# Kernel optimization log

Hardware: AMD Instinct MI355X
Metric: run time of the kernel (lower is better)

Reference implementation:

```python
import jax, jax.numpy as jnp
from jax import lax
import numpy as np

B, T, I, H = 256, 1024, 128, 256


def setup_inputs() -> dict:
    key = jax.random.key(0)
    k1, k2, k3 = jax.random.split(key, 3)
    # Xavier-ish scaling so sigmoid/tanh gates are not saturated
    s_ih = float(np.sqrt(2.0 / (I + 3 * H)))
    s_hh = float(np.sqrt(2.0 / (H + 3 * H)))
    return {
        "x": jax.random.normal(k1, (B, T, I), dtype=jnp.float32),
        "h0": jnp.zeros((B, H), dtype=jnp.float32),
        "weight_ih": jax.random.normal(k2, (3 * H, I), dtype=jnp.float32) * s_ih,
        "weight_hh": jax.random.normal(k3, (3 * H, H), dtype=jnp.float32) * s_hh,
        "bias_ih": jnp.zeros((3 * H,), dtype=jnp.float32),
        "bias_hh": jnp.zeros((3 * H,), dtype=jnp.float32),
    }


def reference(x, h0, weight_ih, weight_hh, bias_ih, bias_hh):
    # Precompute batched input-to-hidden GEMM for all timesteps: [B, T, 3H]
    gates_x = jnp.einsum("bti,gi->btg", x, weight_ih) + bias_ih
    gates_x = jnp.swapaxes(gates_x, 0, 1)  # [T, B, 3H] for scan

    def step(h, gx):
        # NOTE: faithful to source — reset gate multiplies the FULL new-gate
        # preactivation (which already includes the hidden contribution),
        # unlike a standard GRU.
        gates = gx + h @ weight_hh.T + bias_hh  # [B, 3H]
        r, z, n = jnp.split(gates, 3, axis=-1)
        r = jax.nn.sigmoid(r)
        z = jax.nn.sigmoid(z)
        n = jnp.tanh(r * n)
        h_new = (1.0 - z) * h + z * n
        return h_new, h_new

    h_last, outs = lax.scan(step, h0, gates_x)  # outs: [T, B, H]
    output = jnp.swapaxes(outs, 0, 1)  # [B, T, H] (batch_first=True)
    return output, h_last
```

## Files before the change

kernel.cpp:

```cpp
#include <hip/hip_runtime.h>


#define B_SZ 256
#define T_SZ 1024
#define H_SZ 256
#define G3   768
#define NGRP 64
#define SPIN_MAX (1 << 27)
#define HROW 288

typedef __attribute__((ext_vector_type(2))) float f32x2;

template<int CTRL>
__device__ __forceinline__ float dppx(float s) {
    return __int_as_float(
        __builtin_amdgcn_update_dpp(0, __float_as_int(s), CTRL, 0xF, 0xF, true));
}
template<int MASK>
__device__ __forceinline__ float swzx(float s) {
    return __int_as_float(__builtin_amdgcn_ds_swizzle(__float_as_int(s), MASK));
}
__device__ __forceinline__ f32x2 pkfma(f32x2 a, f32x2 b, f32x2 c) {
    f32x2 d;
    asm("v_pk_fma_f32 %0, %1, %2, %3" : "=v"(d) : "v"(a), "v"(b), "v"(c));
    return d;
}

static __device__ __forceinline__ int hpos(int k) { return k + 4 * (k >> 5); }

static __device__ __forceinline__ size_t xsl(int g, int par, int n, int u) {
    return (((size_t)g * 2 + par) * 4 + n) * 256 + u;
}

__global__ void prep_kernel(const float* __restrict__ h0,
                            unsigned long long* __restrict__ xch) {
    int tid = blockIdx.x * blockDim.x + threadIdx.x;
    if (tid < B_SZ * H_SZ) {
        int b = tid >> 8, u = tid & 255;
        int g = b >> 2, n = b & 3;
        unsigned long long val = (unsigned long long)__float_as_uint(h0[tid]);
        xch[xsl(g, 0, n, u)] = val;
        xch[xsl(g, 1, n, u)] = val;
    }
}

__global__ __launch_bounds__(256) void gemm_x_kernel(
    const float* __restrict__ x, const float* __restrict__ wih,
    float* __restrict__ gx, int c, int tcShift)
{
    __shared__ __align__(16) float xs[64][132];
    __shared__ __align__(16) float ws[128][68];
    const int TC = 1 << tcShift;
    const int t  = threadIdx.x;
    const int bx = blockIdx.x, by = blockIdx.y;

#pragma unroll
    for (int i = 0; i < 8; ++i) {
        int f4 = t + i * 256;
        int r  = f4 >> 5, c4 = (f4 & 31) * 4;
        int rho = bx * 64 + r;
        int b = rho >> tcShift, u = rho & (TC - 1);
        float4 v = *(const float4*)(x + ((size_t)b * T_SZ + (size_t)c * TC + u) * 128 + c4);
        *(float4*)&xs[r][c4] = v;
    }

    const int gl = t & 31;
    const int rl = t >> 5;
    float acc[8][4];
#pragma unroll
    for (int i = 0; i < 8; ++i)
#pragma unroll
        for (int jj = 0; jj < 4; ++jj) acc[i][jj] = 0.f;

    for (int kb = 0; kb < 2; ++kb) {
        __syncthreads();
#pragma unroll
        for (int i = 0; i < 8; ++i) {
            int f4 = t + i * 256;
            int row = f4 >> 4, c4 = (f4 & 15) * 4;
            float4 v = *(const float4*)(wih + (size_t)(by * 128 + row) * 128 + kb * 64 + c4);
            *(float4*)&ws[row][c4] = v;
        }
        __syncthreads();

#pragma unroll 4
        for (int k4 = 0; k4 < 16; ++k4) {
            float4 wv0 = *(const float4*)&ws[gl     ][k4 * 4];
            float4 wv1 = *(const float4*)&ws[gl + 32][k4 * 4];
            float4 wv2 = *(const float4*)&ws[gl + 64][k4 * 4];
            float4 wv3 = *(const float4*)&ws[gl + 96][k4 * 4];
#pragma unroll
            for (int rr = 0; rr < 8; ++rr) {
                float4 xv = *(const float4*)&xs[rl + rr * 8][kb * 64 + k4 * 4];
                acc[rr][0] = fmaf(xv.w, wv0.w, fmaf(xv.z, wv0.z, fmaf(xv.y, wv0.y, fmaf(xv.x, wv0.x, acc[rr][0]))));
                acc[rr][1] = fmaf(xv.w, wv1.w, fmaf(xv.z, wv1.z, fmaf(xv.y, wv1.y, fmaf(xv.x, wv1.x, acc[rr][1]))));
                acc[rr][2] = fmaf(xv.w, wv2.w, fmaf(xv.z, wv2.z, fmaf(xv.y, wv2.y, fmaf(xv.x, wv2.x, acc[rr][2]))));
                acc[rr][3] = fmaf(xv.w, wv3.w, fmaf(xv.z, wv3.z, fmaf(xv.y, wv3.y, fmaf(xv.x, wv3.x, acc[rr][3]))));
            }
        }
    }

#pragma unroll
    for (int rr = 0; rr < 8; ++rr) {
        size_t base = (size_t)(bx * 64 + rl + rr * 8) * G3 + by * 128 + gl;
#pragma unroll
        for (int gi = 0; gi < 4; ++gi)
            gx[base + 32 * gi] = acc[rr][gi];
    }
}

#define PIN2(v) asm volatile("" : "+v"(v));

__global__ __launch_bounds__(512)
__attribute__((amdgpu_waves_per_eu(2, 2)))
void gru_kernel(
    const float* __restrict__ gx, const float* __restrict__ whh,
    const float* __restrict__ bih, const float* __restrict__ bhh,
    unsigned long long* __restrict__ xch, float* __restrict__ out,
    int gbase, int tc, int isLast)
{
    __shared__ __align__(16) float hl[4][HROW];
    __shared__ __align__(16) float hst[4][64];

    const int t   = threadIdx.x;
    const int bid = blockIdx.x;
    const int g   = bid & 63;
    const int m   = bid >> 6;
    const int u0  = m * 64;
    const int q   = t >> 5;
    const int p   = t & 31;
    const int pb  = p & 3;
    const int uq  = u0 + 4 * q;
    const int k0  = 8 * p;

    f32x2 wf[12][4];
#pragma unroll
    for (int gate = 0; gate < 3; ++gate) {
#pragma unroll
        for (int e = 0; e < 4; ++e) {
            const float* wr = whh + (size_t)(gate * 256 + uq + e) * H_SZ + k0;
            float4 va = *(const float4*)(wr);
            float4 vb = *(const float4*)(wr + 4);
            wf[gate * 4 + e][0] = (f32x2){va.x, va.y};
            wf[gate * 4 + e][1] = (f32x2){va.z, va.w};
            wf[gate * 4 + e][2] = (f32x2){vb.x, vb.y};
            wf[gate * 4 + e][3] = (f32x2){vb.z, vb.w};
        }
    }
#pragma unroll
    for (int f = 0; f < 12; ++f) {
        PIN2(wf[f][0]) PIN2(wf[f][1]) PIN2(wf[f][2]) PIN2(wf[f][3])
    }

    const bool hi  = (p >= 16);
    const bool act = (p < 4) || (p >= 16 && p < 20);
    const int  ueA = uq + (hi ? 2 : 0);
    float bsrA = 0.f, bszA = 0.f, bsnA = 0.f, bsrB = 0.f, bszB = 0.f, bsnB = 0.f;
    const float* gxp = nullptr;
    if (act) {
        bsrA = bih[ueA]       + bhh[ueA];
        bszA = bih[256 + ueA] + bhh[256 + ueA];
        bsnA = bih[512 + ueA] + bhh[512 + ueA];
        bsrB = bih[ueA + 1]       + bhh[ueA + 1];
        bszB = bih[257 + ueA]     + bhh[257 + ueA];
        bsnB = bih[513 + ueA]     + bhh[513 + ueA];
        gxp = gx + ((size_t)(4 * g + pb) * tc) * G3 + ueA;
    }

    const int n_t  = t >> 7;
    const int c2   = t & 127;
    const int wofs = 2 * c2 + 4 * (c2 >> 4);
    const int Wd = hpos(k0);
    const float* hrow[4];
#pragma unroll
    for (int i = 0; i < 4; ++i) hrow[i] = &hl[i ^ pb][Wd];
    const int pua = hpos(ueA);
    const int n_o = t >> 4, f_o = t & 15;

    float gxrA = 0.f, gxzA = 0.f, gxnA = 0.f, gxrB = 0.f, gxzB = 0.f, gxnB = 0.f;
    if (act) {
        gxrA = gxp[0]; gxzA = gxp[256]; gxnA = gxp[512];
        gxrB = gxp[1]; gxzB = gxp[257]; gxnB = gxp[513];
    }

#pragma unroll 1
    for (int u = 0; u < tc; ++u) {
        const int tg  = gbase + u;
        const int par = tg & 1;

        if (u > 0 && t < 64) {
            float4 o;
            o.x = hst[n_o][4 * f_o];     o.y = hst[n_o][4 * f_o + 1];
            o.z = hst[n_o][4 * f_o + 2]; o.w = hst[n_o][4 * f_o + 3];
            *(float4*)(out + ((size_t)(4 * g + n_o) * T_SZ + (tg - 1)) * H_SZ + u0 + 4 * f_o) = o;
        }

        {
            unsigned long long* sb = xch + xsl(g, par, n_t, 2 * c2);
            const unsigned want = (unsigned)tg;
            unsigned long long v0, v1;
            int sp = 0;
            for (;;) {
                v0 = __hip_atomic_load(sb + 0, __ATOMIC_RELAXED, __HIP_MEMORY_SCOPE_AGENT);
                v1 = __hip_atomic_load(sb + 1, __ATOMIC_RELAXED, __HIP_MEMORY_SCOPE_AGENT);
                bool ok = ((unsigned)(v0 >> 32) == want) & ((unsigned)(v1 >> 32) == want);
                if (ok || ++sp >= SPIN_MAX) break;
                __builtin_amdgcn_s_sleep(1);
            }
            float2 hv;
            hv.x = __uint_as_float((unsigned)v0);
            hv.y = __uint_as_float((unsigned)v1);
            *(float2*)&hl[n_t][wofs] = hv;
        }
        __syncthreads();

        float pgrA = 0.f, pgzA = 0.f, pgnA = 0.f, pgrB = 0.f, pgzB = 0.f, pgnB = 0.f;
        if (act && u + 1 < tc) {
            size_t go = (size_t)(u + 1) * G3;
            pgrA = gxp[go];     pgzA = gxp[go + 256]; pgnA = gxp[go + 512];
            pgrB = gxp[go + 1]; pgzB = gxp[go + 257]; pgnB = gxp[go + 513];
        }

        float s[12][4];
#pragma unroll
        for (int i = 0; i < 4; ++i) {
            const float* hr = hrow[i];
            float4 hv0 = *(const float4*)(hr);
            float4 hv1 = *(const float4*)(hr + 4);
            f32x2 h0 = (f32x2){hv0.x, hv0.y};
            f32x2 h1 = (f32x2){hv0.z, hv0.w};
            f32x2 h2 = (f32x2){hv1.x, hv1.y};
            f32x2 h3 = (f32x2){hv1.z, hv1.w};
            f32x2 z  = (f32x2){0.f, 0.f};
#pragma unroll
            for (int f = 0; f < 12; ++f) {
                f32x2 a = pkfma(h0, wf[f][0],
                          pkfma(h1, wf[f][1],
                          pkfma(h2, wf[f][2],
                          pkfma(h3, wf[f][3], z))));
                s[f][i] = a.x + a.y;
            }
        }

#pragma unroll
        for (int f = 0; f < 12; ++f) {
            s[f][0] += dppx<0xB1>(s[f][1]);
            s[f][2] += dppx<0xB1>(s[f][3]);
            s[f][0] += dppx<0x4E>(s[f][2]);
            s[f][0] += dppx<0x124>(s[f][0]);
            s[f][0] += dppx<0x128>(s[f][0]);
            s[f][0] += swzx<0x401F>(s[f][0]);
        }

        if (act) {
            float srA = hi ? s[2][0]  : s[0][0];
            float srB = hi ? s[3][0]  : s[1][0];
            float szA = hi ? s[6][0]  : s[4][0];
            float szB = hi ? s[7][0]  : s[5][0];
            float snA = hi ? s[10][0] : s[8][0];
            float snB = hi ? s[11][0] : s[9][0];

            float holdA = hl[pb][pua];
            float holdB = hl[pb][pua + 1];
            float arA = srA + gxrA + bsrA;
            float azA = szA + gxzA + bszA;
            float anA = snA + gxnA + bsnA;
            float arB = srB + gxrB + bsrB;
            float azB = szB + gxzB + bszB;
            float anB = snB + gxnB + bsnB;
            float rA = 1.f / (1.f + expf(-arA));
            float zA = 1.f / (1.f + expf(-azA));
            float nA = tanhf(rA * anA);
            float rB = 1.f / (1.f + expf(-arB));
            float zB = 1.f / (1.f + expf(-azB));
            float nB = tanhf(rB * anB);
            float hnA = (1.f - zA) * holdA + zA * nA;
            float hnB = (1.f - zB) * holdB + zB * nB;

            hst[pb][ueA - u0]     = hnA;
            hst[pb][ueA - u0 + 1] = hnB;
            const unsigned long long ver = (unsigned long long)(unsigned)(tg + 1) << 32;
            const int par1 = (tg + 1) & 1;
            __hip_atomic_store(xch + xsl(g, par1, pb, ueA),
                               ver | (unsigned long long)__float_as_uint(hnA),
                               __ATOMIC_RELAXED, __HIP_MEMORY_SCOPE_AGENT);
            __hip_atomic_store(xch + xsl(g, par1, pb, ueA + 1),
                               ver | (unsigned long long)__float_as_uint(hnB),
                               __ATOMIC_RELAXED, __HIP_MEMORY_SCOPE_AGENT);
        }
        gxrA = pgrA; gxzA = pgzA; gxnA = pgnA;
        gxrB = pgrB; gxzB = pgzB; gxnB = pgnB;
        __syncthreads();
    }

    if (t < 64) {
        float4 o;
        o.x = hst[n_o][4 * f_o];     o.y = hst[n_o][4 * f_o + 1];
        o.z = hst[n_o][4 * f_o + 2]; o.w = hst[n_o][4 * f_o + 3];
        *(float4*)(out + ((size_t)(4 * g + n_o) * T_SZ + (gbase + tc - 1)) * H_SZ + u0 + 4 * f_o) = o;
        if (isLast)
            *(float4*)(out + (size_t)B_SZ * T_SZ * H_SZ
                           + (size_t)(4 * g + n_o) * H_SZ + u0 + 4 * f_o) = o;
    }
}

extern "C" void kernel_launch(void* const* d_in, const int* in_sizes, int n_in,
                              void* d_out, int out_size, void* d_ws, size_t ws_size,
                              hipStream_t stream) {
    const float* x   = (const float*)d_in[0];
    const float* h0  = (const float*)d_in[1];
    const float* wih = (const float*)d_in[2];
    const float* whh = (const float*)d_in[3];
    const float* bih = (const float*)d_in[4];
    const float* bhh = (const float*)d_in[5];
    float* out = (float*)d_out;

    char* ws = (char*)d_ws;
    const size_t xchB = (size_t)NGRP * 2 * 4 * 256 * 8;
    unsigned long long* xch = (unsigned long long*)ws;
    float* gxb = (float*)(ws + xchB);

    int tcShift = 10;
    while (tcShift > 0 &&
           xchB + (786432ull << tcShift) > ws_size) --tcShift;
    const int TC  = 1 << tcShift;
    const int nCh = T_SZ / TC;

    prep_kernel<<<dim3(256), dim3(256), 0, stream>>>(h0, xch);
    for (int c = 0; c < nCh; ++c) {
        gemm_x_kernel<<<dim3(B_SZ * TC / 64, 6), dim3(256), 0, stream>>>(
            x, wih, gxb, c, tcShift);
        gru_kernel<<<dim3(B_SZ), dim3(512), 0, stream>>>(
            gxb, whh, bih, bhh, xch, out, c * TC, TC, (c == nCh - 1) ? 1 : 0);
    }
}
```

Measured before the change: 3.642 ms.

## Split batch group into two half-groups to overlap exchange wait with compute

Each workgroup's four batch rows are split into two pairs (A and B) processed in sequence within each timestep. Each pair waits only on its own exchanged hidden-state slots, so pair A's matvec and gate math can run while pair B's values from other blocks are still arriving. The cost is an extra __syncthreads and spin-wait per step, plus a reduction layout that now activates 4 of every 32 lanes instead of 8 for the gate math.

New measurement: 4.893 ms. +34.4%, slower.

```diff
diff --git a/kernel.cpp b/kernel.cpp
--- a/kernel.cpp
+++ b/kernel.cpp
@@ -119,7 +119,8 @@
     unsigned long long* __restrict__ xch, float* __restrict__ out,
     int gbase, int tc, int isLast)
 {
-    __shared__ __align__(16) float hl[4][HROW];
+    __shared__ __align__(16) float hlA[2][HROW];
+    __shared__ __align__(16) float hlB[2][HROW];
     __shared__ __align__(16) float hst[4][64];
 
     const int t   = threadIdx.x;
@@ -129,7 +130,6 @@
     const int u0  = m * 64;
     const int q   = t >> 5;
     const int p   = t & 31;
-    const int pb  = p & 3;
     const int uq  = u0 + 4 * q;
     const int k0  = 8 * p;
 
@@ -152,41 +152,54 @@
         PIN2(wf[f][0]) PIN2(wf[f][1]) PIN2(wf[f][2]) PIN2(wf[f][3])
     }
 
-    const bool hi  = (p >= 16);
-    const bool act = (p < 4) || (p >= 16 && p < 20);
-    const int  ueA = uq + (hi ? 2 : 0);
-    float bsrA = 0.f, bszA = 0.f, bsnA = 0.f, bsrB = 0.f, bszB = 0.f, bsnB = 0.f;
-    const float* gxp = nullptr;
+    const int  nb  = p & 1;
+    const int  hi  = (p >> 1) & 1;
+    const bool act = (p < 4);
+    const int  ueA = uq + 2 * hi;
+    float bsr0 = 0.f, bsz0 = 0.f, bsn0 = 0.f, bsr1 = 0.f, bsz1 = 0.f, bsn1 = 0.f;
+    const float* gxpA = nullptr;
+    const float* gxpB = nullptr;
     if (act) {
-        bsrA = bih[ueA]       + bhh[ueA];
-        bszA = bih[256 + ueA] + bhh[256 + ueA];
-        bsnA = bih[512 + ueA] + bhh[512 + ueA];
-        bsrB = bih[ueA + 1]       + bhh[ueA + 1];
-        bszB = bih[257 + ueA]     + bhh[257 + ueA];
-        bsnB = bih[513 + ueA]     + bhh[513 + ueA];
-        gxp = gx + ((size_t)(4 * g + pb) * tc) * G3 + ueA;
-    }
-
-    const int n_t  = t >> 7;
-    const int c2   = t & 127;
-    const int wofs = 2 * c2 + 4 * (c2 >> 4);
+        bsr0 = bih[ueA]       + bhh[ueA];
+        bsz0 = bih[256 + ueA] + bhh[256 + ueA];
+        bsn0 = bih[512 + ueA] + bhh[512 + ueA];
+        bsr1 = bih[ueA + 1]   + bhh[ueA + 1];
+        bsz1 = bih[257 + ueA] + bhh[257 + ueA];
+        bsn1 = bih[513 + ueA] + bhh[513 + ueA];
+        gxpA = gx + ((size_t)(4 * g + nb) * tc) * G3 + ueA;
+        gxpB = gx + ((size_t)(4 * g + 2 + nb) * tc) * G3 + ueA;
+    }
+
+    const int n_loc = t >> 8;
+    const int un    = t & 255;
+    const int wofs  = hpos(un);
     const int Wd = hpos(k0);
-    const float* hrow[4];
-#pragma unroll
-    for (int i = 0; i < 4; ++i) hrow[i] = &hl[i ^ pb][Wd];
+    const float* hrA[2];
+    const float* hrB[2];
+#pragma unroll
+    for (int i = 0; i < 2; ++i) {
+        hrA[i] = &hlA[i ^ nb][Wd];
+        hrB[i] = &hlB[i ^ nb][Wd];
+    }
     const int pua = hpos(ueA);
     const int n_o = t >> 4, f_o = t & 15;
 
-    float gxrA = 0.f, gxzA = 0.f, gxnA = 0.f, gxrB = 0.f, gxzB = 0.f, gxnB = 0.f;
+    float gArA = 0.f, gAzA = 0.f, gAnA = 0.f, gArB = 0.f, gAzB = 0.f, gAnB = 0.f;
+    float gBrA = 0.f, gBzA = 0.f, gBnA = 0.f, gBrB = 0.f, gBzB = 0.f, gBnB = 0.f;
     if (act) {
-        gxrA = gxp[0]; gxzA = gxp[256]; gxnA = gxp[512];
-        gxrB = gxp[1]; gxzB = gxp[257]; gxnB = gxp[513];
+        gArA = gxpA[0]; gAzA = gxpA[256]; gAnA = gxpA[512];
+        gArB = gxpA[1]; gAzB = gxpA[257]; gAnB = gxpA[513];
+        gBrA = gxpB[0]; gBzA = gxpB[256]; gBnA = gxpB[512];
+        gBrB = gxpB[1]; gBzB = gxpB[257]; gBnB = gxpB[513];
     }
 
 #pragma unroll 1
     for (int u = 0; u < tc; ++u) {
-        const int tg  = gbase + u;
-        const int par = tg & 1;
+        const int tg   = gbase + u;
+        const int par  = tg & 1;
+        const int par1 = (tg + 1) & 1;
+        const unsigned long long ver =
+            (unsigned long long)(unsigned)(tg + 1) << 32;
 
         if (u > 0 && t < 64) {
             float4 o;
@@ -196,100 +209,174 @@
         }
 
         {
-            unsigned long long* sb = xch + xsl(g, par, n_t, 2 * c2);
+            unsigned long long* sb = xch + xsl(g, par, n_loc, un);
             const unsigned want = (unsigned)tg;
-            unsigned long long v0, v1;
+            unsigned long long v = __hip_atomic_load(sb, __ATOMIC_RELAXED, __HIP_MEMORY_SCOPE_AGENT);
             int sp = 0;
-            for (;;) {
-                v0 = __hip_atomic_load(sb + 0, __ATOMIC_RELAXED, __HIP_MEMORY_SCOPE_AGENT);
-                v1 = __hip_atomic_load(sb + 1, __ATOMIC_RELAXED, __HIP_MEMORY_SCOPE_AGENT);
-                bool ok = ((unsigned)(v0 >> 32) == want) & ((unsigned)(v1 >> 32) == want);
-                if (ok || ++sp >= SPIN_MAX) break;
+            while ((unsigned)(v >> 32) != want && ++sp < SPIN_MAX) {
                 __builtin_amdgcn_s_sleep(1);
-            }
-            float2 hv;
-            hv.x = __uint_as_float((unsigned)v0);
-            hv.y = __uint_as_float((unsigned)v1);
-            *(float2*)&hl[n_t][wofs] = hv;
+                v = __hip_atomic_load(sb, __ATOMIC_RELAXED, __HIP_MEMORY_SCOPE_AGENT);
+            }
+            hlA[n_loc][wofs] = __uint_as_float((unsigned)v);
         }
         __syncthreads();
 
-        float pgrA = 0.f, pgzA = 0.f, pgnA = 0.f, pgrB = 0.f, pgzB = 0.f, pgnB = 0.f;
+        float pArA = 0.f, pAzA = 0.f, pAnA = 0.f, pArB = 0.f, pAzB = 0.f, pAnB = 0.f;
         if (act && u + 1 < tc) {
             size_t go = (size_t)(u + 1) * G3;
-            pgrA = gxp[go];     pgzA = gxp[go + 256]; pgnA = gxp[go + 512];
-            pgrB = gxp[go + 1]; pgzB = gxp[go + 257]; pgnB = gxp[go + 513];
-        }
-
-        float s[12][4];
-#pragma unroll
-        for (int i = 0; i < 4; ++i) {
-            const float* hr = hrow[i];
-            float4 hv0 = *(const float4*)(hr);
-            float4 hv1 = *(const float4*)(hr + 4);
-            f32x2 h0 = (f32x2){hv0.x, hv0.y};
-            f32x2 h1 = (f32x2){hv0.z, hv0.w};
-            f32x2 h2 = (f32x2){hv1.x, hv1.y};
-            f32x2 h3 = (f32x2){hv1.z, hv1.w};
-            f32x2 z  = (f32x2){0.f, 0.f};
+            pArA = gxpA[go];     pAzA = gxpA[go + 256]; pAnA = gxpA[go + 512];
+            pArB = gxpA[go + 1]; pAzB = gxpA[go + 257]; pAnB = gxpA[go + 513];
+        }
+
+        {
+            float s[12][2];
+#pragma unroll
+            for (int i = 0; i < 2; ++i) {
+                const float* hr = hrA[i];
+                float4 hv0 = *(const float4*)(hr);
+                float4 hv1 = *(const float4*)(hr + 4);
+                f32x2 h0 = (f32x2){hv0.x, hv0.y};
+                f32x2 h1 = (f32x2){hv0.z, hv0.w};
+                f32x2 h2 = (f32x2){hv1.x, hv1.y};
+                f32x2 h3 = (f32x2){hv1.z, hv1.w};
+                f32x2 z  = (f32x2){0.f, 0.f};
+#pragma unroll
+                for (int f = 0; f < 12; ++f) {
+                    f32x2 a = pkfma(h0, wf[f][0],
+                              pkfma(h1, wf[f][1],
+                              pkfma(h2, wf[f][2],
+                              pkfma(h3, wf[f][3], z))));
+                    s[f][i] = a.x + a.y;
+                }
+            }
 #pragma unroll
             for (int f = 0; f < 12; ++f) {
-                f32x2 a = pkfma(h0, wf[f][0],
-                          pkfma(h1, wf[f][1],
-                          pkfma(h2, wf[f][2],
-                          pkfma(h3, wf[f][3], z))));
-                s[f][i] = a.x + a.y;
-            }
-        }
-
-#pragma unroll
-        for (int f = 0; f < 12; ++f) {
-            s[f][0] += dppx<0xB1>(s[f][1]);
-            s[f][2] += dppx<0xB1>(s[f][3]);
-            s[f][0] += dppx<0x4E>(s[f][2]);
-            s[f][0] += dppx<0x124>(s[f][0]);
-            s[f][0] += dppx<0x128>(s[f][0]);
-            s[f][0] += swzx<0x401F>(s[f][0]);
-        }
-
-        if (act) {
-            float srA = hi ? s[2][0]  : s[0][0];
-            float srB = hi ? s[3][0]  : s[1][0];
-            float szA = hi ? s[6][0]  : s[4][0];
-            float szB = hi ? s[7][0]  : s[5][0];
-            float snA = hi ? s[10][0] : s[8][0];
-            float snB = hi ? s[11][0] : s[9][0];
-
-            float holdA = hl[pb][pua];
-            float holdB = hl[pb][pua + 1];
-            float arA = srA + gxrA + bsrA;
-            float azA = szA + gxzA + bszA;
-            float anA = snA + gxnA + bsnA;
-            float arB = srB + gxrB + bsrB;
-            float azB = szB + gxzB + bszB;
-            float anB = snB + gxnB + bsnB;
-            float rA = 1.f / (1.f + expf(-arA));
-            float zA = 1.f / (1.f + expf(-azA));
-            float nA = tanhf(rA * anA);
-            float rB = 1.f / (1.f + expf(-arB));
-            float zB = 1.f / (1.f + expf(-azB));
-            float nB = tanhf(rB * anB);
-            float hnA = (1.f - zA) * holdA + zA * nA;
-            float hnB = (1.f - zB) * holdB + zB * nB;
-
-            hst[pb][ueA - u0]     = hnA;
-            hst[pb][ueA - u0 + 1] = hnB;
-            const unsigned long long ver = (unsigned long long)(unsigned)(tg + 1) << 32;
-            const int par1 = (tg + 1) & 1;
-            __hip_atomic_store(xch + xsl(g, par1, pb, ueA),
-                               ver | (unsigned long long)__float_as_uint(hnA),
-                               __ATOMIC_RELAXED, __HIP_MEMORY_SCOPE_AGENT);
-            __hip_atomic_store(xch + xsl(g, par1, pb, ueA + 1),
-                               ver | (unsigned long long)__float_as_uint(hnB),
-                               __ATOMIC_RELAXED, __HIP_MEMORY_SCOPE_AGENT);
-        }
-        gxrA = pgrA; gxzA = pgzA; gxnA = pgnA;
-        gxrB = pgrB; gxzB = pgzB; gxnB = pgnB;
+                s[f][0] += dppx<0xB1>(s[f][1]);
+                s[f][0] += dppx<0x4E>(s[f][0]);
+                s[f][0] += dppx<0x124>(s[f][0]);
+                s[f][0] += dppx<0x128>(s[f][0]);
+                s[f][0] += swzx<0x401F>(s[f][0]);
+            }
+            if (act) {
+                float srA = hi ? s[2][0]  : s[0][0];
+                float srB = hi ? s[3][0]  : s[1][0];
+                float szA = hi ? s[6][0]  : s[4][0];
+                float szB = hi ? s[7][0]  : s[5][0];
+                float snA = hi ? s[10][0] : s[8][0];
+                float snB = hi ? s[11][0] : s[9][0];
+                float holdA = hlA[nb][pua];
+                float holdB = hlA[nb][pua + 1];
+                float arA = srA + gArA + bsr0;
+                float azA = szA + gAzA + bsz0;
+                float anA = snA + gAnA + bsn0;
+                float arB = srB + gArB + bsr1;
+                float azB = szB + gAzB + bsz1;
+                float anB = snB + gAnB + bsn1;
+                float rA = 1.f / (1.f + expf(-arA));
+                float zA = 1.f / (1.f + expf(-azA));
+                float nA = tanhf(rA * anA);
+                float rB = 1.f / (1.f + expf(-arB));
+                float zB = 1.f / (1.f + expf(-azB));
+                float nB = tanhf(rB * anB);
+                float hnA = (1.f - zA) * holdA + zA * nA;
+                float hnB = (1.f - zB) * holdB + zB * nB;
+                hst[nb][ueA - u0]     = hnA;
+                hst[nb][ueA - u0 + 1] = hnB;
+                __hip_atomic_store(xch + xsl(g, par1, nb, ueA),
+                                   ver | (unsigned long long)__float_as_uint(hnA),
+                                   __ATOMIC_RELAXED, __HIP_MEMORY_SCOPE_AGENT);
+                __hip_atomic_store(xch + xsl(g, par1, nb, ueA + 1),
+                                   ver | (unsigned long long)__float_as_uint(hnB),
+                                   __ATOMIC_RELAXED, __HIP_MEMORY_SCOPE_AGENT);
+            }
+            gArA = pArA; gAzA = pAzA; gAnA = pAnA;
+            gArB = pArB; gAzB = pAzB; gAnB = pAnB;
+        }
+
+        {
+            unsigned long long* sb = xch + xsl(g, par, 2 + n_loc, un);
+            const unsigned want = (unsigned)tg;
+            unsigned long long v = __hip_atomic_load(sb, __ATOMIC_RELAXED, __HIP_MEMORY_SCOPE_AGENT);
+            int sp = 0;
+            while ((unsigned)(v >> 32) != want && ++sp < SPIN_MAX) {
+                __builtin_amdgcn_s_sleep(1);
+                v = __hip_atomic_load(sb, __ATOMIC_RELAXED, __HIP_MEMORY_SCOPE_AGENT);
+            }
+            hlB[n_loc][wofs] = __uint_as_float((unsigned)v);
+        }
+        __syncthreads();
+
+        float pBrA = 0.f, pBzA = 0.f, pBnA = 0.f, pBrB = 0.f, pBzB = 0.f, pBnB = 0.f;
+        if (act && u + 1 < tc) {
+            size_t go = (size_t)(u + 1) * G3;
+            pBrA = gxpB[go];     pBzA = gxpB[go + 256]; pBnA = gxpB[go + 512];
+            pBrB = gxpB[go + 1]; pBzB = gxpB[go + 257]; pBnB = gxpB[go + 513];
+        }
+
+        {
+            float s[12][2];
+#pragma unroll
+            for (int i = 0; i < 2; ++i) {
+                const float* hr = hrB[i];
+                float4 hv0 = *(const float4*)(hr);
+                float4 hv1 = *(const float4*)(hr + 4);
+                f32x2 h0 = (f32x2){hv0.x, hv0.y};
+                f32x2 h1 = (f32x2){hv0.z, hv0.w};
+                f32x2 h2 = (f32x2){hv1.x, hv1.y};
+                f32x2 h3 = (f32x2){hv1.z, hv1.w};
+                f32x2 z  = (f32x2){0.f, 0.f};
+#pragma unroll
+                for (int f = 0; f < 12; ++f) {
+                    f32x2 a = pkfma(h0, wf[f][0],
+                              pkfma(h1, wf[f][1],
+                              pkfma(h2, wf[f][2],
+                              pkfma(h3, wf[f][3], z))));
+                    s[f][i] = a.x + a.y;
+                }
+            }
+#pragma unroll
+            for (int f = 0; f < 12; ++f) {
+                s[f][0] += dppx<0xB1>(s[f][1]);
+                s[f][0] += dppx<0x4E>(s[f][0]);
+                s[f][0] += dppx<0x124>(s[f][0]);
+                s[f][0] += dppx<0x128>(s[f][0]);
+                s[f][0] += swzx<0x401F>(s[f][0]);
+            }
+            if (act) {
+                float srA = hi ? s[2][0]  : s[0][0];
+                float srB = hi ? s[3][0]  : s[1][0];
+                float szA = hi ? s[6][0]  : s[4][0];
+                float szB = hi ? s[7][0]  : s[5][0];
+                float snA = hi ? s[10][0] : s[8][0];
+                float snB = hi ? s[11][0] : s[9][0];
+                float holdA = hlB[nb][pua];
+                float holdB = hlB[nb][pua + 1];
+                float arA = srA + gBrA + bsr0;
+                float azA = szA + gBzA + bsz0;
+                float anA = snA + gBnA + bsn0;
+                float arB = srB + gBrB + bsr1;
+                float azB = szB + gBzB + bsz1;
+                float anB = snB + gBnB + bsn1;
+                float rA = 1.f / (1.f + expf(-arA));
+                float zA = 1.f / (1.f + expf(-azA));
+                float nA = tanhf(rA * anA);
+                float rB = 1.f / (1.f + expf(-arB));
+                float zB = 1.f / (1.f + expf(-azB));
+                float nB = tanhf(rB * anB);
+                float hnA = (1.f - zA) * holdA + zA * nA;
+                float hnB = (1.f - zB) * holdB + zB * nB;
+                hst[2 + nb][ueA - u0]     = hnA;
+                hst[2 + nb][ueA - u0 + 1] = hnB;
+                __hip_atomic_store(xch + xsl(g, par1, 2 + nb, ueA),
+                                   ver | (unsigned long long)__float_as_uint(hnA),
+                                   __ATOMIC_RELAXED, __HIP_MEMORY_SCOPE_AGENT);
+                __hip_atomic_store(xch + xsl(g, par1, 2 + nb, ueA + 1),
+                                   ver | (unsigned long long)__float_as_uint(hnB),
+                                   __ATOMIC_RELAXED, __HIP_MEMORY_SCOPE_AGENT);
+            }
+            gBrA = pBrA; gBzA = pBzA; gBnA = pBnA;
+            gBrB = pBrB; gBzB = pBzB; gBnB = pBnB;
+        }
         __syncthreads();
     }
 
```

## Double-buffer hidden state in LDS to drop per-step barrier and spread gate work

Applied to the files above, without the earlier changes.

Hidden-state and output staging buffers in LDS are double-buffered by timestep parity, which removes the second __syncthreads per recurrence step. The gate epilogue now spreads across 16 lanes per wave, each handling one hidden unit, where before 8 lanes each handled two units, so the serial transcendental chain per step is shorter. The output store moves to after the barrier and reads the previous parity buffer. The spin-wait cap is also lowered. Correctness now depends on the cross-block version handshake ordering LDS reuse two steps apart.

New measurement: 3.712 ms. About the same (+1.9%).

```diff
diff --git a/kernel.cpp b/kernel.cpp
--- a/kernel.cpp
+++ b/kernel.cpp
@@ -6,7 +6,7 @@
 #define H_SZ 256
 #define G3   768
 #define NGRP 64
-#define SPIN_MAX (1 << 27)
+#define SPIN_MAX (1 << 21)
 #define HROW 288
 
 typedef __attribute__((ext_vector_type(2))) float f32x2;
@@ -119,8 +119,8 @@
     unsigned long long* __restrict__ xch, float* __restrict__ out,
     int gbase, int tc, int isLast)
 {
-    __shared__ __align__(16) float hl[4][HROW];
-    __shared__ __align__(16) float hst[4][64];
+    __shared__ __align__(16) float hl[2][4][HROW];
+    __shared__ __align__(16) float hst[2][4][64];
 
     const int t   = threadIdx.x;
     const int bid = blockIdx.x;
@@ -152,48 +152,33 @@
         PIN2(wf[f][0]) PIN2(wf[f][1]) PIN2(wf[f][2]) PIN2(wf[f][3])
     }
 
-    const bool hi  = (p >= 16);
-    const bool act = (p < 4) || (p >= 16 && p < 20);
-    const int  ueA = uq + (hi ? 2 : 0);
-    float bsrA = 0.f, bszA = 0.f, bsnA = 0.f, bsrB = 0.f, bszB = 0.f, bsnB = 0.f;
+    const bool act = (p < 16);
+    const int  e   = (p >> 2) & 3;
+    const int  ue  = uq + e;
+    float bsr = 0.f, bsz = 0.f, bsn = 0.f;
     const float* gxp = nullptr;
     if (act) {
-        bsrA = bih[ueA]       + bhh[ueA];
-        bszA = bih[256 + ueA] + bhh[256 + ueA];
-        bsnA = bih[512 + ueA] + bhh[512 + ueA];
-        bsrB = bih[ueA + 1]       + bhh[ueA + 1];
-        bszB = bih[257 + ueA]     + bhh[257 + ueA];
-        bsnB = bih[513 + ueA]     + bhh[513 + ueA];
-        gxp = gx + ((size_t)(4 * g + pb) * tc) * G3 + ueA;
+        bsr = bih[ue]       + bhh[ue];
+        bsz = bih[256 + ue] + bhh[256 + ue];
+        bsn = bih[512 + ue] + bhh[512 + ue];
+        gxp = gx + ((size_t)(4 * g + pb) * tc) * G3 + ue;
     }
 
     const int n_t  = t >> 7;
     const int c2   = t & 127;
     const int wofs = 2 * c2 + 4 * (c2 >> 4);
     const int Wd = hpos(k0);
-    const float* hrow[4];
-#pragma unroll
-    for (int i = 0; i < 4; ++i) hrow[i] = &hl[i ^ pb][Wd];
-    const int pua = hpos(ueA);
+    const int pue = hpos(ue);
     const int n_o = t >> 4, f_o = t & 15;
 
-    float gxrA = 0.f, gxzA = 0.f, gxnA = 0.f, gxrB = 0.f, gxzB = 0.f, gxnB = 0.f;
-    if (act) {
-        gxrA = gxp[0]; gxzA = gxp[256]; gxnA = gxp[512];
-        gxrB = gxp[1]; gxzB = gxp[257]; gxnB = gxp[513];
-    }
+    float gxr = 0.f, gxz = 0.f, gxn = 0.f;
+    if (act) { gxr = gxp[0]; gxz = gxp[256]; gxn = gxp[512]; }
 
 #pragma unroll 1
     for (int u = 0; u < tc; ++u) {
-        const int tg  = gbase + u;
-        const int par = tg & 1;
-
-        if (u > 0 && t < 64) {
-            float4 o;
-            o.x = hst[n_o][4 * f_o];     o.y = hst[n_o][4 * f_o + 1];
-            o.z = hst[n_o][4 * f_o + 2]; o.w = hst[n_o][4 * f_o + 3];
-            *(float4*)(out + ((size_t)(4 * g + n_o) * T_SZ + (tg - 1)) * H_SZ + u0 + 4 * f_o) = o;
-        }
+        const int tg   = gbase + u;
+        const int par  = tg & 1;
+        const int par1 = (tg + 1) & 1;
 
         {
             unsigned long long* sb = xch + xsl(g, par, n_t, 2 * c2);
@@ -210,35 +195,44 @@
             float2 hv;
             hv.x = __uint_as_float((unsigned)v0);
             hv.y = __uint_as_float((unsigned)v1);
-            *(float2*)&hl[n_t][wofs] = hv;
+            *(float2*)&hl[par][n_t][wofs] = hv;
         }
         __syncthreads();
 
-        float pgrA = 0.f, pgzA = 0.f, pgnA = 0.f, pgrB = 0.f, pgzB = 0.f, pgnB = 0.f;
+        if (u > 0 && t < 64) {
+            float4 o;
+            o.x = hst[par1][n_o][4 * f_o];     o.y = hst[par1][n_o][4 * f_o + 1];
+            o.z = hst[par1][n_o][4 * f_o + 2]; o.w = hst[par1][n_o][4 * f_o + 3];
+            *(float4*)(out + ((size_t)(4 * g + n_o) * T_SZ + (tg - 1)) * H_SZ + u0 + 4 * f_o) = o;
+        }
+
+        float pgr = 0.f, pgz = 0.f, pgn = 0.f;
         if (act && u + 1 < tc) {
             size_t go = (size_t)(u + 1) * G3;
-            pgrA = gxp[go];     pgzA = gxp[go + 256]; pgnA = gxp[go + 512];
-            pgrB = gxp[go + 1]; pgzB = gxp[go + 257]; pgnB = gxp[go + 513];
+            pgr = gxp[go]; pgz = gxp[go + 256]; pgn = gxp[go + 512];
         }
 
         float s[12][4];
-#pragma unroll
-        for (int i = 0; i < 4; ++i) {
-            const float* hr = hrow[i];
-            float4 hv0 = *(const float4*)(hr);
-            float4 hv1 = *(const float4*)(hr + 4);
-            f32x2 h0 = (f32x2){hv0.x, hv0.y};
-            f32x2 h1 = (f32x2){hv0.z, hv0.w};
-            f32x2 h2 = (f32x2){hv1.x, hv1.y};
-            f32x2 h3 = (f32x2){hv1.z, hv1.w};
-            f32x2 z  = (f32x2){0.f, 0.f};
-#pragma unroll
-            for (int f = 0; f < 12; ++f) {
-                f32x2 a = pkfma(h0, wf[f][0],
-                          pkfma(h1, wf[f][1],
-                          pkfma(h2, wf[f][2],
-                          pkfma(h3, wf[f][3], z))));
-                s[f][i] = a.x + a.y;
+        {
+            const float* hb = &hl[par][0][0] + Wd;
+#pragma unroll
+            for (int i = 0; i < 4; ++i) {
+                const float* hr = hb + (size_t)(i ^ pb) * HROW;
+                float4 hv0 = *(const float4*)(hr);
+                float4 hv1 = *(const float4*)(hr + 4);
+                f32x2 h0 = (f32x2){hv0.x, hv0.y};
+                f32x2 h1 = (f32x2){hv0.z, hv0.w};
+                f32x2 h2 = (f32x2){hv1.x, hv1.y};
+                f32x2 h3 = (f32x2){hv1.z, hv1.w};
+                f32x2 z  = (f32x2){0.f, 0.f};
+#pragma unroll
+                for (int f = 0; f < 12; ++f) {
+                    f32x2 a = pkfma(h0, wf[f][0],
+                              pkfma(h1, wf[f][1],
+                              pkfma(h2, wf[f][2],
+                              pkfma(h3, wf[f][3], z))));
+                    s[f][i] = a.x + a.y;
+                }
             }
         }
 
@@ -253,54 +247,43 @@
         }
 
         if (act) {
-            float srA = hi ? s[2][0]  : s[0][0];
-            float srB = hi ? s[3][0]  : s[1][0];
-            float szA = hi ? s[6][0]  : s[4][0];
-            float szB = hi ? s[7][0]  : s[5][0];
-            float snA = hi ? s[10][0] : s[8][0];
-            float snB = hi ? s[11][0] : s[9][0];
-
-            float holdA = hl[pb][pua];
-            float holdB = hl[pb][pua + 1];
-            float arA = srA + gxrA + bsrA;
-            float azA = szA + gxzA + bszA;
-            float anA = snA + gxnA + bsnA;
-            float arB = srB + gxrB + bsrB;
-            float azB = szB + gxzB + bszB;
-            float anB = snB + gxnB + bsnB;
-            float rA = 1.f / (1.f + expf(-arA));
-            float zA = 1.f / (1.f + expf(-azA));
-            float nA = tanhf(rA * anA);
-            float rB = 1.f / (1.f + expf(-arB));
-            float zB = 1.f / (1.f + expf(-azB));
-            float nB = tanhf(rB * anB);
-            float hnA = (1.f - zA) * holdA + zA * nA;
-            float hnB = (1.f - zB) * holdB + zB * nB;
-
-            hst[pb][ueA - u0]     = hnA;
-            hst[pb][ueA - u0 + 1] = hnB;
-            const unsigned long long ver = (unsigned long long)(unsigned)(tg + 1) << 32;
-            const int par1 = (tg + 1) & 1;
-            __hip_atomic_store(xch + xsl(g, par1, pb, ueA),
-                               ver | (unsigned long long)__float_as_uint(hnA),
+            float sr = (e & 2) ? ((e & 1) ? s[3][0]  : s[2][0])
+                               : ((e & 1) ? s[1][0]  : s[0][0]);
+            float sz = (e & 2) ? ((e & 1) ? s[7][0]  : s[6][0])
+                               : ((e & 1) ? s[5][0]  : s[4][0]);
+            float sn = (e & 2) ? ((e & 1) ? s[11][0] : s[10][0])
+                               : ((e & 1) ? s[9][0]  : s[8][0]);
+
+            float hold = hl[par][pb][pue];
+            float ar = sr + gxr + bsr;
+            float az = sz + gxz + bsz;
+            float an = sn + gxn + bsn;
+            float r  = 1.f / (1.f + expf(-ar));
+            float z  = 1.f / (1.f + expf(-az));
+            float nn = tanhf(r * an);
+            float hn = (1.f - z) * hold + z * nn;
+
+            hst[par][pb][ue - u0] = hn;
+            __hip_atomic_store(xch + xsl(g, par1, pb, ue),
+                               ((unsigned long long)(unsigned)(tg + 1) << 32) |
+                               (unsigned long long)__float_as_uint(hn),
                                __ATOMIC_RELAXED, __HIP_MEMORY_SCOPE_AGENT);
-            __hip_atomic_store(xch + xsl(g, par1, pb, ueA + 1),
-                               ver | (unsigned long long)__float_as_uint(hnB),
-                               __ATOMIC_RELAXED, __HIP_MEMORY_SCOPE_AGENT);
-        }
-        gxrA = pgrA; gxzA = pgzA; gxnA = pgnA;
-        gxrB = pgrB; gxzB = pgzB; gxnB = pgnB;
-        __syncthreads();
-    }
-
-    if (t < 64) {
-        float4 o;
-        o.x = hst[n_o][4 * f_o];     o.y = hst[n_o][4 * f_o + 1];
-        o.z = hst[n_o][4 * f_o + 2]; o.w = hst[n_o][4 * f_o + 3];
-        *(float4*)(out + ((size_t)(4 * g + n_o) * T_SZ + (gbase + tc - 1)) * H_SZ + u0 + 4 * f_o) = o;
-        if (isLast)
-            *(float4*)(out + (size_t)B_SZ * T_SZ * H_SZ
-                           + (size_t)(4 * g + n_o) * H_SZ + u0 + 4 * f_o) = o;
+        }
+        gxr = pgr; gxz = pgz; gxn = pgn;
+    }
+
+    __syncthreads();
+    {
+        const int fpar = (gbase + tc - 1) & 1;
+        if (t < 64) {
+            float4 o;
+            o.x = hst[fpar][n_o][4 * f_o];     o.y = hst[fpar][n_o][4 * f_o + 1];
+            o.z = hst[fpar][n_o][4 * f_o + 2]; o.w = hst[fpar][n_o][4 * f_o + 3];
+            *(float4*)(out + ((size_t)(4 * g + n_o) * T_SZ + (gbase + tc - 1)) * H_SZ + u0 + 4 * f_o) = o;
+            if (isLast)
+                *(float4*)(out + (size_t)B_SZ * T_SZ * H_SZ
+                               + (size_t)(4 * g + n_o) * H_SZ + u0 + 4 * f_o) = o;
+        }
     }
 }
 
```
